# Kernel tuning notes

Measured on AMD Instinct MI355X. Metric: run time of the kernel, lower is better.

## Reference

```python
import jax, jax.numpy as jnp
import numpy as np

N_NODES = 100000
N_EDGES = 3200000
IN_DIM, HID, N_LAB = 128, 64, 121


def setup_inputs() -> dict:
    key = jax.random.key(0)
    ks = jax.random.split(key, 8)
    x = jax.random.normal(ks[0], (N_NODES, IN_DIM), dtype=jnp.float32)
    edge_index = jax.random.randint(ks[1], (2, N_EDGES), 0, N_NODES, dtype=jnp.int64)
    W1 = jax.random.normal(ks[2], (IN_DIM, HID), dtype=jnp.float32) * (1.0 / np.sqrt(IN_DIM))
    b1 = jnp.zeros((HID,), dtype=jnp.float32)
    W2 = jax.random.normal(ks[3], (HID, HID), dtype=jnp.float32) * (1.0 / np.sqrt(HID))
    b2 = jnp.zeros((HID,), dtype=jnp.float32)
    Wout = jax.random.normal(ks[4], (HID, N_LAB), dtype=jnp.float32) * (1.0 / np.sqrt(HID))
    bout = jnp.zeros((N_LAB,), dtype=jnp.float32)
    return {"x": x, "edge_index": edge_index, "W1": W1, "b1": b1,
            "W2": W2, "b2": b2, "Wout": Wout, "bout": bout}


def _gcn_conv(x, W, b, src, dst, norm, n):
    # x' = D^{-1/2}(A+I)D^{-1/2} X W + b  (edges already include self-loops)
    xw = x @ W                                   # [N, out]
    msg = xw[src] * norm[:, None]                # [E+N, out] gather + scale
    agg = jax.ops.segment_sum(msg, dst, num_segments=n)  # scatter-add
    return agg + b


def reference(x, edge_index, W1, b1, W2, b2, Wout, bout):
    n = x.shape[0]
    loop = jnp.arange(n, dtype=edge_index.dtype)
    src = jnp.concatenate([edge_index[0], loop])
    dst = jnp.concatenate([edge_index[1], loop])
    # symmetric normalization (self-loops guarantee deg >= 1)
    deg = jax.ops.segment_sum(jnp.ones_like(dst, dtype=x.dtype), dst, num_segments=n)
    dinv = jax.lax.rsqrt(deg)
    norm = dinv[src] * dinv[dst]                 # [E+N]

    h = jax.nn.relu(_gcn_conv(x, W1, b1, src, dst, norm, n))
    # dropout p=0.5 is identity in eval mode (training=False)
    h = jax.nn.relu(_gcn_conv(h, W2, b2, src, dst, norm, n))
    logits = h @ Wout + bout                     # [N, num_labels]
    return logits
```

## Files before the change

### kernel.cpp

```cpp
#include <hip/hip_runtime.h>
#include <hip/hip_bf16.h>
#include <hip/hip_fp16.h>


#define IN_DIM 128
#define HID 64
#define N_LAB 121
#define NB_BLK 512

__global__ void scan1(const int* __restrict__ in, int* __restrict__ out,
                      int* __restrict__ bsums, int n) {
    __shared__ int s[256];
    int i = blockIdx.x * 256 + threadIdx.x;
    int v = (i < n) ? in[i] : 0;
    s[threadIdx.x] = v;
    __syncthreads();
    for (int off = 1; off < 256; off <<= 1) {
        int t = (threadIdx.x >= off) ? s[threadIdx.x - off] : 0;
        __syncthreads();
        s[threadIdx.x] += t;
        __syncthreads();
    }
    if (i < n) out[i] = s[threadIdx.x] - v;
    if (threadIdx.x == 255) bsums[blockIdx.x] = s[255];
}

__global__ __launch_bounds__(512) void bucket_count(const int* __restrict__ dst,
                                                    int* __restrict__ counts,
                                                    int nbuk, int chunk, int E) {
    __shared__ int c[512];
    for (int j = threadIdx.x; j < nbuk; j += 512) c[j] = 0;
    __syncthreads();
    int beg = blockIdx.x * chunk;
    int end = min(beg + chunk, E);
    int n = end - beg;
    if (n > 0) {
        const int2* p2 = (const int2*)(dst + beg);
        int nPair = n >> 1;
        for (int t = threadIdx.x; t < nPair; t += 512) {
            int2 d = p2[t];
            atomicAdd(&c[d.x >> 8], 1);
            atomicAdd(&c[d.y >> 8], 1);
        }
        if ((n & 1) && threadIdx.x == 0)
            atomicAdd(&c[dst[end - 1] >> 8], 1);
    }
    __syncthreads();
    for (int j = threadIdx.x; j < nbuk; j += 512)
        counts[j * NB_BLK + blockIdx.x] = c[j];
}

__device__ __forceinline__ void pair_scan_1024(const int* __restrict__ bsums,
                                               int* ps, int* bscan, int nb) {
    const int t = threadIdx.x;
    int pa = (2 * t     < nb) ? bsums[2 * t]     : 0;
    int pb = (2 * t + 1 < nb) ? bsums[2 * t + 1] : 0;
    ps[t] = pa + pb;
    __syncthreads();
    for (int off = 1; off < 512; off <<= 1) {
        int v = (t >= off) ? ps[t - off] : 0;
        __syncthreads();
        ps[t] += v;
        __syncthreads();
    }
    int excl = ps[t] - (pa + pb);
    bscan[2 * t]     = excl;
    bscan[2 * t + 1] = excl + pa;
    __syncthreads();
}

__global__ __launch_bounds__(512) void bucket_scatter(const int* __restrict__ src,
                                                      const int* __restrict__ dst,
                                                      const int* __restrict__ base,
                                                      const int* __restrict__ bsums,
                                                      int* __restrict__ bucketed,
                                                      int nbuk, int nbM,
                                                      int chunk, int E) {
    __shared__ int c[512];
    __shared__ int bs[512];
    __shared__ int ps[512];
    __shared__ int bscan[1024];
    pair_scan_1024(bsums, ps, bscan, nbM);
    for (int j = threadIdx.x; j < nbuk; j += 512) {
        c[j] = 0;
        int idx = j * NB_BLK + blockIdx.x;
        bs[j] = base[idx] + bscan[idx >> 8];
    }
    __syncthreads();
    int beg = blockIdx.x * chunk;
    int end = min(beg + chunk, E);
    int n = end - beg;
    if (n > 0) {
        const int2* d2 = (const int2*)(dst + beg);
        const int2* s2 = (const int2*)(src + beg);
        int nPair = n >> 1;
        for (int t = threadIdx.x; t < nPair; t += 512) {
            int2 d = d2[t];
            int2 s = s2[t];
            int b0 = d.x >> 8;
            int r0 = atomicAdd(&c[b0], 1);
            bucketed[bs[b0] + r0] = ((d.x & 255) << 17) | s.x;
            int b1 = d.y >> 8;
            int r1 = atomicAdd(&c[b1], 1);
            bucketed[bs[b1] + r1] = ((d.y & 255) << 17) | s.y;
        }
        if ((n & 1) && threadIdx.x == 0) {
            int d = dst[end - 1];
            int b = d >> 8;
            int r = atomicAdd(&c[b], 1);
            bucketed[bs[b] + r] = ((d & 255) << 17) | src[end - 1];
        }
    }
}

__global__ __launch_bounds__(512) void bucket_sort(const int* __restrict__ bucketed,
                                                   const int* __restrict__ base,
                                                   const int* __restrict__ bsums,
                                                   int* __restrict__ srcs,
                                                   int* __restrict__ row_ptr,
                                                   float* __restrict__ dinv,
                                                   int nbuk, int nbM, int N, int E) {
    __shared__ int h[512];
    __shared__ int cur[256];
    __shared__ int ps[512];
    __shared__ int bscan[1024];
    pair_scan_1024(bsums, ps, bscan, nbM);
    int b = blockIdx.x;
    int nodeBase = b << 8;
    int idx0 = b * NB_BLK;
    int s = base[idx0] + bscan[idx0 >> 8];
    int e;
    if (b == nbuk - 1) {
        e = E;
    } else {
        int idx1 = (b + 1) * NB_BLK;
        e = base[idx1] + bscan[idx1 >> 8];
    }
    h[threadIdx.x] = 0;
    __syncthreads();
    for (int i = s + threadIdx.x; i < e; i += 512)
        atomicAdd(&h[bucketed[i] >> 17], 1);
    __syncthreads();
    int v = h[threadIdx.x];
    for (int off = 1; off < 512; off <<= 1) {
        int t = (threadIdx.x >= off) ? h[threadIdx.x - off] : 0;
        __syncthreads();
        h[threadIdx.x] += t;
        __syncthreads();
    }
    if (threadIdx.x < 256) {
        int excl = h[threadIdx.x] - v;
        cur[threadIdx.x] = excl;
        int node = nodeBase + threadIdx.x;
        if (node < N) {
            row_ptr[node] = s + excl;
            dinv[node] = rsqrtf((float)v + 1.0f);
        }
    }
    if (b == nbuk - 1 && threadIdx.x == 0) row_ptr[N] = E;
    __syncthreads();
    for (int i = s + threadIdx.x; i < e; i += 512) {
        int p = bucketed[i];
        int d = p >> 17;
        int r = atomicAdd(&cur[d], 1);
        srcs[s + r] = (p & 0x1FFFF) << 7;
    }
}

template <int K, int N, int ROWS, typename OT>
__global__ __launch_bounds__(256) void gemm_kernel(
        const float* __restrict__ A, const float* __restrict__ B,
        const float* __restrict__ bias, const float* __restrict__ rowscale,
        OT* __restrict__ C, int M) {
    constexpr int NPAD = (N <= 64) ? 64 : 128;
    constexpr int CG = NPAD / 4;
    constexpr int RG = 256 / CG;
    constexpr int RPT = ROWS / RG;
    constexpr int KT = 32;
    constexpr int APAD = KT + 4;
    __shared__ float Bs[K * NPAD];
    __shared__ float As[ROWS * APAD];

    for (int i = threadIdx.x; i < K * NPAD; i += 256) {
        int c = i & (NPAD - 1);
        int k = i / NPAD;
        Bs[i] = (c < N) ? B[k * N + c] : 0.f;
    }

    const int cg = threadIdx.x % CG;
    const int rg = threadIdx.x / CG;
    const int row_base = blockIdx.x * ROWS;

    float acc[RPT][4];
    #pragma unroll
    for (int j = 0; j < RPT; ++j) {
        acc[j][0] = 0.f; acc[j][1] = 0.f; acc[j][2] = 0.f; acc[j][3] = 0.f;
    }

    for (int kt = 0; kt < K; kt += KT) {
        __syncthreads();
        for (int v = threadIdx.x; v < ROWS * (KT / 4); v += 256) {
            int r  = v >> 3;
            int c4 = v & 7;
            int gr = row_base + r;
            if (gr > M - 1) gr = M - 1;
            *(float4*)&As[r * APAD + c4 * 4] =
                *(const float4*)&A[(size_t)gr * K + kt + c4 * 4];
        }
        __syncthreads();
        for (int k = 0; k < KT; k += 4) {
            float4 Bq[4];
            #pragma unroll
            for (int kk = 0; kk < 4; ++kk)
                Bq[kk] = *(const float4*)&Bs[(kt + k + kk) * NPAD + cg * 4];
            #pragma unroll
            for (int j = 0; j < RPT; ++j) {
                const float4 Aq = *(const float4*)&As[(rg + RG * j) * APAD + k];
                #pragma unroll
                for (int c = 0; c < 4; ++c) {
                    const float b0 = ((const float*)&Bq[0])[c];
                    const float b1 = ((const float*)&Bq[1])[c];
                    const float b2 = ((const float*)&Bq[2])[c];
                    const float b3 = ((const float*)&Bq[3])[c];
                    float a = acc[j][c];
                    a = fmaf(Aq.x, b0, a);
                    a = fmaf(Aq.y, b1, a);
                    a = fmaf(Aq.z, b2, a);
                    a = fmaf(Aq.w, b3, a);
                    acc[j][c] = a;
                }
            }
        }
    }

    float bv[4];
    #pragma unroll
    for (int c = 0; c < 4; ++c) {
        int col = cg * 4 + c;
        bv[c] = (bias && col < N) ? bias[col] : 0.f;
    }

    #pragma unroll
    for (int j = 0; j < RPT; ++j) {
        const int r = row_base + rg + RG * j;
        if (r >= M) continue;
        const float sc = rowscale ? rowscale[r] : 1.0f;
        float o[4];
        #pragma unroll
        for (int c = 0; c < 4; ++c) o[c] = fmaf(acc[j][c], sc, bv[c]);
        OT* Crow = C + (size_t)r * N;
        if constexpr (sizeof(OT) == 4 && (N % 4 == 0)) {
            *(float4*)&Crow[cg * 4] = make_float4(o[0], o[1], o[2], o[3]);
        } else if constexpr (sizeof(OT) == 2 && (N % 4 == 0)) {
            __half2* p = (__half2*)&Crow[cg * 4];
            p[0] = __floats2half2_rn(o[0], o[1]);
            p[1] = __floats2half2_rn(o[2], o[3]);
        } else {
            #pragma unroll
            for (int c = 0; c < 4; ++c) {
                int col = cg * 4 + c;
                if (col < N) Crow[col] = (OT)o[c];
            }
        }
    }
}

__global__ __launch_bounds__(256) void aggregate(
        const __half* __restrict__ feat2, const int* __restrict__ rp,
        const int* __restrict__ srcs, const float* __restrict__ dinv,
        const float* __restrict__ bias, float* __restrict__ out, int N) {
    const int wid = (int)((((size_t)blockIdx.x * 256) + threadIdx.x) >> 6);
    if (wid >= N) return;
    const int lane = threadIdx.x & 63;
    const int slot = lane >> 3;
    const int oct  = lane & 7;
    const char* fbB = (const char*)feat2 + oct * 16;

    float acc[8];
    #pragma unroll
    for (int i = 0; i < 8; ++i) acc[i] = 0.f;

    if (slot == 0) {
        const uint4 q = *(const uint4*)(fbB + ((size_t)wid << 7));
        const __half2* h = (const __half2*)&q;
        #pragma unroll
        for (int i = 0; i < 4; ++i) {
            const float2 f = __half22float2(h[i]);
            acc[2 * i]     += f.x;
            acc[2 * i + 1] += f.y;
        }
    }

    const int beg = rp[wid], end = rp[wid + 1];
    int idx = beg + slot;
    while (__any(idx < end)) {
        const bool p0 = idx < end;
        const bool p1 = (idx + 8) < end;
        const int i0 = p0 ? idx : beg;
        const int i1 = p1 ? (idx + 8) : beg;
        const int o0 = srcs[i0];
        const int o1 = srcs[i1];
        uint4 q0 = *(const uint4*)(fbB + o0);
        uint4 q1 = *(const uint4*)(fbB + o1);
        if (!p0) { q0.x = 0u; q0.y = 0u; q0.z = 0u; q0.w = 0u; }
        if (!p1) { q1.x = 0u; q1.y = 0u; q1.z = 0u; q1.w = 0u; }
        const __half2* h0 = (const __half2*)&q0;
        const __half2* h1 = (const __half2*)&q1;
        #pragma unroll
        for (int i = 0; i < 4; ++i) {
            const float2 f0 = __half22float2(h0[i]);
            const float2 f1 = __half22float2(h1[i]);
            acc[2 * i]     += f0.x + f1.x;
            acc[2 * i + 1] += f0.y + f1.y;
        }
        idx += 16;
    }

    #pragma unroll
    for (int m = 8; m <= 32; m <<= 1) {
        #pragma unroll
        for (int i = 0; i < 8; ++i)
            acc[i] += __shfl_xor(acc[i], m, 64);
    }

    if (slot == 0) {
        const float sc = dinv[wid];
        float o[8];
        #pragma unroll
        for (int i = 0; i < 8; ++i)
            o[i] = fmaxf(fmaf(acc[i], sc, bias[oct * 8 + i]), 0.f);
        float4* d4 = (float4*)(out + (((size_t)wid << 6) + oct * 8));
        d4[0] = make_float4(o[0], o[1], o[2], o[3]);
        d4[1] = make_float4(o[4], o[5], o[6], o[7]);
    }
}

extern "C" void kernel_launch(void* const* d_in, const int* in_sizes, int n_in,
                              void* d_out, int out_size, void* d_ws, size_t ws_size,
                              hipStream_t stream) {
    const float* x    = (const float*)d_in[0];
    const int*   ei   = (const int*)d_in[1];
    const float* W1   = (const float*)d_in[2];
    const float* b1   = (const float*)d_in[3];
    const float* W2   = (const float*)d_in[4];
    const float* b2   = (const float*)d_in[5];
    const float* Wout = (const float*)d_in[6];
    const float* bout = (const float*)d_in[7];
    float* out = (float*)d_out;

    const int N = in_sizes[0] / IN_DIM;
    const int E = in_sizes[1] / 2;
    const int* srcI = ei;
    const int* dstI = ei + E;

    const int nbuk = (N + 255) >> 8;
    const int M1 = nbuk * NB_BLK;
    const int chunk = (E + NB_BLK - 1) / NB_BLK;

    int*    row_ptr = (int*)d_ws;
    float*  dinv    = (float*)(row_ptr + (N + 1));
    int*    counts  = (int*)(dinv + N);
    int*    base    = counts + M1;
    int*    bsums   = base + M1;
    int*    srcs    = bsums + 1024;
    __half* feat2   = (__half*)(((uintptr_t)(srcs + E) + 15) & ~(uintptr_t)15);
    float*  hbuf    = (float*)(feat2 + (size_t)N * HID);
    int*    bucketed = (int*)feat2;

    const int nbM = (M1 + 255) / 256;
    const int gemmBlocks128 = (N + 127) / 128;
    const int gemmBlocks64  = (N + 63) / 64;
    const int aggBlocks = (int)(((size_t)N * HID + 255) / 256);

    bucket_count<<<NB_BLK, 512, 0, stream>>>(dstI, counts, nbuk, chunk, E);
    scan1<<<nbM, 256, 0, stream>>>(counts, base, bsums, M1);
    bucket_scatter<<<NB_BLK, 512, 0, stream>>>(srcI, dstI, base, bsums,
                                               bucketed, nbuk, nbM, chunk, E);
    bucket_sort<<<nbuk, 512, 0, stream>>>(bucketed, base, bsums, srcs, row_ptr,
                                          dinv, nbuk, nbM, N, E);

    gemm_kernel<IN_DIM, HID, 128, __half><<<gemmBlocks128, 256, 0, stream>>>(
        x, W1, nullptr, dinv, feat2, N);
    aggregate<<<aggBlocks, 256, 0, stream>>>(feat2, row_ptr, srcs, dinv, b1, hbuf, N);

    gemm_kernel<HID, HID, 128, __half><<<gemmBlocks128, 256, 0, stream>>>(
        hbuf, W2, nullptr, dinv, feat2, N);
    aggregate<<<aggBlocks, 256, 0, stream>>>(feat2, row_ptr, srcs, dinv, b2, hbuf, N);

    gemm_kernel<HID, N_LAB, 64, float><<<gemmBlocks64, 256, 0, stream>>>(
        hbuf, Wout, bout, nullptr, out, N);
}
```

Baseline: 480.9 us.

## Fuse CSR bucket-sort kernels into one persistent kernel with grid barriers

Merges the four preprocessing kernels (count, scan, scatter, per-bucket sort) into a single 512-block kernel that uses atomic-counter grid barriers between phases, and restructures the scan as per-bucket rows of 512 so the second-level scan is done redundantly per block. This removes three kernel launches and their gaps. In exchange it relies on all 512 blocks of 512 threads being co-resident for the spin barriers, which risks deadlock if occupancy is insufficient, and adds an extra memset launch. Chunk is also rounded to even so the int2 loads stay aligned.

```diff
diff --git a/kernel.cpp b/kernel.cpp
--- a/kernel.cpp
+++ b/kernel.cpp
@@ -8,162 +8,151 @@
 #define N_LAB 121
 #define NB_BLK 512
 
-__global__ void scan1(const int* __restrict__ in, int* __restrict__ out,
-                      int* __restrict__ bsums, int n) {
-    __shared__ int s[256];
-    int i = blockIdx.x * 256 + threadIdx.x;
-    int v = (i < n) ? in[i] : 0;
-    s[threadIdx.x] = v;
-    __syncthreads();
-    for (int off = 1; off < 256; off <<= 1) {
-        int t = (threadIdx.x >= off) ? s[threadIdx.x - off] : 0;
-        __syncthreads();
-        s[threadIdx.x] += t;
-        __syncthreads();
-    }
-    if (i < n) out[i] = s[threadIdx.x] - v;
-    if (threadIdx.x == 255) bsums[blockIdx.x] = s[255];
-}
-
-__global__ __launch_bounds__(512) void bucket_count(const int* __restrict__ dst,
-                                                    int* __restrict__ counts,
-                                                    int nbuk, int chunk, int E) {
-    __shared__ int c[512];
-    for (int j = threadIdx.x; j < nbuk; j += 512) c[j] = 0;
-    __syncthreads();
-    int beg = blockIdx.x * chunk;
-    int end = min(beg + chunk, E);
-    int n = end - beg;
-    if (n > 0) {
-        const int2* p2 = (const int2*)(dst + beg);
-        int nPair = n >> 1;
-        for (int t = threadIdx.x; t < nPair; t += 512) {
-            int2 d = p2[t];
-            atomicAdd(&c[d.x >> 8], 1);
-            atomicAdd(&c[d.y >> 8], 1);
-        }
-        if ((n & 1) && threadIdx.x == 0)
-            atomicAdd(&c[dst[end - 1] >> 8], 1);
-    }
-    __syncthreads();
-    for (int j = threadIdx.x; j < nbuk; j += 512)
-        counts[j * NB_BLK + blockIdx.x] = c[j];
-}
-
-__device__ __forceinline__ void pair_scan_1024(const int* __restrict__ bsums,
-                                               int* ps, int* bscan, int nb) {
+__device__ __forceinline__ void gridbar(int* ctr, int target) {
+    __syncthreads();
+    if (threadIdx.x == 0) {
+        __threadfence();
+        atomicAdd(ctr, 1);
+        while (atomicAdd(ctr, 0) < target) {
+            __builtin_amdgcn_s_sleep(8);
+        }
+        __threadfence();
+    }
+    __syncthreads();
+}
+
+__global__ __launch_bounds__(512) void fused_sort(
+        const int* __restrict__ src, const int* __restrict__ dst,
+        int* __restrict__ counts, int* __restrict__ lexcl,
+        int* __restrict__ bsums, int* __restrict__ bucketed,
+        int* __restrict__ srcs, int* __restrict__ row_ptr,
+        float* __restrict__ dinv, int* __restrict__ bar,
+        int nbuk, int chunk, int E, int N) {
+    __shared__ int smA[512];
+    __shared__ int smB[512];
+    __shared__ int smC[512];
+    __shared__ int smD[1024];
+    const int blk = blockIdx.x;
     const int t = threadIdx.x;
-    int pa = (2 * t     < nb) ? bsums[2 * t]     : 0;
-    int pb = (2 * t + 1 < nb) ? bsums[2 * t + 1] : 0;
-    ps[t] = pa + pb;
-    __syncthreads();
-    for (int off = 1; off < 512; off <<= 1) {
-        int v = (t >= off) ? ps[t - off] : 0;
-        __syncthreads();
-        ps[t] += v;
-        __syncthreads();
-    }
-    int excl = ps[t] - (pa + pb);
-    bscan[2 * t]     = excl;
-    bscan[2 * t + 1] = excl + pa;
-    __syncthreads();
-}
-
-__global__ __launch_bounds__(512) void bucket_scatter(const int* __restrict__ src,
-                                                      const int* __restrict__ dst,
-                                                      const int* __restrict__ base,
-                                                      const int* __restrict__ bsums,
-                                                      int* __restrict__ bucketed,
-                                                      int nbuk, int nbM,
-                                                      int chunk, int E) {
-    __shared__ int c[512];
-    __shared__ int bs[512];
-    __shared__ int ps[512];
-    __shared__ int bscan[1024];
-    pair_scan_1024(bsums, ps, bscan, nbM);
-    for (int j = threadIdx.x; j < nbuk; j += 512) {
-        c[j] = 0;
-        int idx = j * NB_BLK + blockIdx.x;
-        bs[j] = base[idx] + bscan[idx >> 8];
-    }
-    __syncthreads();
-    int beg = blockIdx.x * chunk;
-    int end = min(beg + chunk, E);
-    int n = end - beg;
-    if (n > 0) {
-        const int2* d2 = (const int2*)(dst + beg);
-        const int2* s2 = (const int2*)(src + beg);
-        int nPair = n >> 1;
-        for (int t = threadIdx.x; t < nPair; t += 512) {
-            int2 d = d2[t];
-            int2 s = s2[t];
-            int b0 = d.x >> 8;
-            int r0 = atomicAdd(&c[b0], 1);
-            bucketed[bs[b0] + r0] = ((d.x & 255) << 17) | s.x;
-            int b1 = d.y >> 8;
-            int r1 = atomicAdd(&c[b1], 1);
-            bucketed[bs[b1] + r1] = ((d.y & 255) << 17) | s.y;
-        }
-        if ((n & 1) && threadIdx.x == 0) {
-            int d = dst[end - 1];
-            int b = d >> 8;
-            int r = atomicAdd(&c[b], 1);
-            bucketed[bs[b] + r] = ((d & 255) << 17) | src[end - 1];
-        }
-    }
-}
-
-__global__ __launch_bounds__(512) void bucket_sort(const int* __restrict__ bucketed,
-                                                   const int* __restrict__ base,
-                                                   const int* __restrict__ bsums,
-                                                   int* __restrict__ srcs,
-                                                   int* __restrict__ row_ptr,
-                                                   float* __restrict__ dinv,
-                                                   int nbuk, int nbM, int N, int E) {
-    __shared__ int h[512];
-    __shared__ int cur[256];
-    __shared__ int ps[512];
-    __shared__ int bscan[1024];
-    pair_scan_1024(bsums, ps, bscan, nbM);
-    int b = blockIdx.x;
-    int nodeBase = b << 8;
-    int idx0 = b * NB_BLK;
-    int s = base[idx0] + bscan[idx0 >> 8];
-    int e;
-    if (b == nbuk - 1) {
-        e = E;
-    } else {
-        int idx1 = (b + 1) * NB_BLK;
-        e = base[idx1] + bscan[idx1 >> 8];
-    }
-    h[threadIdx.x] = 0;
-    __syncthreads();
-    for (int i = s + threadIdx.x; i < e; i += 512)
-        atomicAdd(&h[bucketed[i] >> 17], 1);
-    __syncthreads();
-    int v = h[threadIdx.x];
-    for (int off = 1; off < 512; off <<= 1) {
-        int t = (threadIdx.x >= off) ? h[threadIdx.x - off] : 0;
-        __syncthreads();
-        h[threadIdx.x] += t;
-        __syncthreads();
-    }
-    if (threadIdx.x < 256) {
-        int excl = h[threadIdx.x] - v;
-        cur[threadIdx.x] = excl;
-        int node = nodeBase + threadIdx.x;
-        if (node < N) {
-            row_ptr[node] = s + excl;
-            dinv[node] = rsqrtf((float)v + 1.0f);
-        }
-    }
-    if (b == nbuk - 1 && threadIdx.x == 0) row_ptr[N] = E;
-    __syncthreads();
-    for (int i = s + threadIdx.x; i < e; i += 512) {
-        int p = bucketed[i];
-        int d = p >> 17;
-        int r = atomicAdd(&cur[d], 1);
-        srcs[s + r] = (p & 0x1FFFF) << 7;
+    const int beg = blk * chunk;
+    const int end = min(beg + chunk, E);
+
+    for (int j = t; j < nbuk; j += 512) smA[j] = 0;
+    __syncthreads();
+    {
+        int n = end - beg;
+        if (n > 0) {
+            const int2* p2 = (const int2*)(dst + beg);
+            int nPair = n >> 1;
+            for (int i = t; i < nPair; i += 512) {
+                int2 d = p2[i];
+                atomicAdd(&smA[d.x >> 8], 1);
+                atomicAdd(&smA[d.y >> 8], 1);
+            }
+            if ((n & 1) && t == 0) atomicAdd(&smA[dst[end - 1] >> 8], 1);
+        }
+    }
+    __syncthreads();
+    for (int j = t; j < nbuk; j += 512)
+        counts[j * NB_BLK + blk] = smA[j];
+
+    gridbar(&bar[0], gridDim.x);
+
+    if (blk < nbuk) {
+        const int i = blk * 512 + t;
+        const int v = counts[i];
+        smA[t] = v;
+        __syncthreads();
+        for (int off = 1; off < 512; off <<= 1) {
+            int x = (t >= off) ? smA[t - off] : 0;
+            __syncthreads();
+            smA[t] += x;
+            __syncthreads();
+        }
+        lexcl[i] = smA[t] - v;
+        if (t == 511) bsums[blk] = smA[511];
+    }
+    gridbar(&bar[1], gridDim.x);
+
+    {
+        int pa = (2 * t     < nbuk) ? bsums[2 * t]     : 0;
+        int pb = (2 * t + 1 < nbuk) ? bsums[2 * t + 1] : 0;
+        smC[t] = pa + pb;
+        __syncthreads();
+        for (int off = 1; off < 512; off <<= 1) {
+            int x = (t >= off) ? smC[t - off] : 0;
+            __syncthreads();
+            smC[t] += x;
+            __syncthreads();
+        }
+        int excl = smC[t] - (pa + pb);
+        smD[2 * t]     = excl;
+        smD[2 * t + 1] = excl + pa;
+        __syncthreads();
+    }
+    for (int j = t; j < nbuk; j += 512) {
+        smA[j] = 0;
+        smB[j] = lexcl[j * NB_BLK + blk] + smD[j];
+    }
+    __syncthreads();
+    {
+        int n = end - beg;
+        if (n > 0) {
+            const int2* d2 = (const int2*)(dst + beg);
+            const int2* s2 = (const int2*)(src + beg);
+            int nPair = n >> 1;
+            for (int i = t; i < nPair; i += 512) {
+                int2 d = d2[i];
+                int2 s = s2[i];
+                int b0 = d.x >> 8;
+                int r0 = atomicAdd(&smA[b0], 1);
+                bucketed[smB[b0] + r0] = ((d.x & 255) << 17) | s.x;
+                int b1 = d.y >> 8;
+                int r1 = atomicAdd(&smA[b1], 1);
+                bucketed[smB[b1] + r1] = ((d.y & 255) << 17) | s.y;
+            }
+            if ((n & 1) && t == 0) {
+                int d = dst[end - 1];
+                int b = d >> 8;
+                int r = atomicAdd(&smA[b], 1);
+                bucketed[smB[b] + r] = ((d & 255) << 17) | src[end - 1];
+            }
+        }
+    }
+    gridbar(&bar[2], gridDim.x);
+
+    if (blk < nbuk) {
+        const int s0 = smD[blk];
+        const int e0 = (blk == nbuk - 1) ? E : smD[blk + 1];
+        smA[t] = 0;
+        __syncthreads();
+        for (int i = s0 + t; i < e0; i += 512)
+            atomicAdd(&smA[bucketed[i] >> 17], 1);
+        __syncthreads();
+        int v = smA[t];
+        for (int off = 1; off < 512; off <<= 1) {
+            int x = (t >= off) ? smA[t - off] : 0;
+            __syncthreads();
+            smA[t] += x;
+            __syncthreads();
+        }
+        if (t < 256) {
+            int excl = smA[t] - v;
+            smB[t] = excl;
+            int node = (blk << 8) + t;
+            if (node < N) {
+                row_ptr[node] = s0 + excl;
+                dinv[node] = rsqrtf((float)v + 1.0f);
+            }
+        }
+        if (blk == nbuk - 1 && t == 0) row_ptr[N] = E;
+        __syncthreads();
+        for (int i = s0 + t; i < e0; i += 512) {
+            int p = bucketed[i];
+            int d = p >> 17;
+            int r = atomicAdd(&smB[d], 1);
+            srcs[s0 + r] = (p & 0x1FFFF) << 7;
+        }
     }
 }
 
@@ -355,29 +344,28 @@
 
     const int nbuk = (N + 255) >> 8;
     const int M1 = nbuk * NB_BLK;
-    const int chunk = (E + NB_BLK - 1) / NB_BLK;
+    int chunk = (E + NB_BLK - 1) / NB_BLK;
+    chunk = (chunk + 1) & ~1;
 
     int*    row_ptr = (int*)d_ws;
     float*  dinv    = (float*)(row_ptr + (N + 1));
     int*    counts  = (int*)(dinv + N);
-    int*    base    = counts + M1;
-    int*    bsums   = base + M1;
-    int*    srcs    = bsums + 1024;
+    int*    lexcl   = counts + M1;
+    int*    bsums   = lexcl + M1;
+    int*    bar     = bsums + 512;
+    int*    srcs    = bar + 4;
     __half* feat2   = (__half*)(((uintptr_t)(srcs + E) + 15) & ~(uintptr_t)15);
     float*  hbuf    = (float*)(feat2 + (size_t)N * HID);
     int*    bucketed = (int*)feat2;
 
-    const int nbM = (M1 + 255) / 256;
     const int gemmBlocks128 = (N + 127) / 128;
     const int gemmBlocks64  = (N + 63) / 64;
     const int aggBlocks = (int)(((size_t)N * HID + 255) / 256);
 
-    bucket_count<<<NB_BLK, 512, 0, stream>>>(dstI, counts, nbuk, chunk, E);
-    scan1<<<nbM, 256, 0, stream>>>(counts, base, bsums, M1);
-    bucket_scatter<<<NB_BLK, 512, 0, stream>>>(srcI, dstI, base, bsums,
-                                               bucketed, nbuk, nbM, chunk, E);
-    bucket_sort<<<nbuk, 512, 0, stream>>>(bucketed, base, bsums, srcs, row_ptr,
-                                          dinv, nbuk, nbM, N, E);
+    hipMemsetAsync(bar, 0, 4 * sizeof(int), stream);
+    fused_sort<<<NB_BLK, 512, 0, stream>>>(srcI, dstI, counts, lexcl, bsums,
+                                           bucketed, srcs, row_ptr, dinv, bar,
+                                           nbuk, chunk, E, N);
 
     gemm_kernel<IN_DIM, HID, 128, __half><<<gemmBlocks128, 256, 0, stream>>>(
         x, W1, nullptr, dinv, feat2, N);
```

Result: slower. 652.2 us (+35.6%).
